# Optimization experiments

Hardware: AMD Instinct MI355X
Metric: run time of the kernel (lower is better)

## Reference

```python
import jax, jax.numpy as jnp
import numpy as np

N, H2, T = 64, 1024, 512  # num steps/documents, 2*hidden_dim, tokens per step
EPS = 1e-12  # torch F.normalize eps


def setup_inputs() -> dict:
    key = jax.random.key(0)
    k1, k2, k3, k4 = jax.random.split(key, 4)
    return {
        "hidden_states": jax.random.normal(k1, (N, H2, T), dtype=jnp.float32),
        "W_attention": jax.random.normal(k2, (H2, H2), dtype=jnp.float32),
        "bias_attention": jax.random.normal(k3, (H2,), dtype=jnp.float32),
        "u_w0": jax.random.normal(k4, (H2,), dtype=jnp.float32),
    }


def reference(hidden_states, W_attention, bias_attention, u_w0):
    n = hidden_states.shape[0]

    # Sequential recurrence on u_w: u_w <- normalize(u_w @ W^T + b), updated
    # BEFORE being used at each step i. Collect the post-update value per step.
    def step(u, _):
        u_new = u @ W_attention.T + bias_attention
        u_new = u_new / jnp.maximum(jnp.linalg.norm(u_new), EPS)
        return u_new, u_new

    _, u_ws = jax.lax.scan(step, u_w0, None, length=n)  # (N, 2H)

    # u_it = tanh(h_i^T W^T + b) for all steps, batched: (N, T, 2H)
    u_it = jnp.tanh(jnp.einsum('ndt,ed->nte', hidden_states, W_attention)
                    + bias_attention)

    # attention scores per step, softmax over the T axis (torch Softmax(dim=0)
    # on a (T,1) column)
    scores = jnp.einsum('nte,ne->nt', u_it, u_ws)  # (N, T)
    a = jax.nn.softmax(scores, axis=1)

    # weighted sum s_i = h_i @ a_i -> stacked as rows: (N, 2H)
    s = jnp.einsum('ndt,nt->nd', hidden_states, a)
    return s
```

## Files before the change

kernel.cpp:

```cpp
#include <hip/hip_runtime.h>
#include <cstdint>
#include <cstddef>

#define H2 1024
#define TT 512
#define NSTEPS 64
#define RBLK 32
#define RTHR 512
#define PREBLK 224
#define TOTBLK 256
#define NTILES 2048u
#define NOUT 512u

using floatx4 = __attribute__((__ext_vector_type__(4))) float;
using half8   = __attribute__((__ext_vector_type__(8))) _Float16;
using half4   = __attribute__((__ext_vector_type__(4))) _Float16;
typedef unsigned long long u64;

__device__ __forceinline__ float tanh_fast(float x) {
  return 1.0f - 2.0f / (__expf(2.0f * x) + 1.0f);
}

#define GLDS16(gp, lp)                                                         \
  __builtin_amdgcn_global_load_lds(                                            \
      (const __attribute__((address_space(1))) void*)(gp),                     \
      (__attribute__((address_space(3))) void*)(lp), 16, 0, 0)

__global__ __launch_bounds__(RTHR, 1) void fused_kernel(
    const float* __restrict__ W, const float* __restrict__ bias,
    const float* __restrict__ u0, float* __restrict__ vbuf,
    float* __restrict__ norm2, _Float16* __restrict__ Wh,
    const float* __restrict__ h, _Float16* __restrict__ hhT,
    float* __restrict__ scores, float* __restrict__ out,
    unsigned* __restrict__ ctrs) {
  __shared__ __align__(16) char smem[98432];
  int tid = threadIdx.x;
  unsigned* done    = ctrs;
  unsigned* queue   = ctrs + 16;
  unsigned* donecnt = ctrs + 32;
  unsigned* outq    = ctrs + 96;

  if (blockIdx.x < RBLK) {
    float* ub = (float*)smem;
    float* bredn = (float*)(smem + 8192);
    int w = tid >> 6, l = tid & 63;
    int r0 = blockIdx.x * RBLK + w * 4;

    floatx4 wreg[16];
    float blv[4];
#pragma unroll
    for (int p = 0; p < 4; ++p) {
      const float* wr = W + ((size_t)(r0 + p) << 10) + 4 * l;
#pragma unroll
      for (int j = 0; j < 4; ++j)
        wreg[p * 4 + j] = *(const floatx4*)(wr + 256 * j);
      blv[p] = bias[r0 + p];
    }
#pragma unroll
    for (int j = 0; j < 16; ++j) asm volatile("" : "+v"(wreg[j]));

    for (int i = 0; i < NSTEPS; ++i) {
      float* cb = ub + (i & 1) * 1024;
      float rs;
      if (i == 0) {
        if (w == 0) {
#pragma unroll
          for (int j = 0; j < 4; ++j) {
            floatx4 v = *((const floatx4*)u0 + l + 64 * j);
            *(floatx4*)(cb + 4 * l + 256 * j) = v;
          }
        }
        __syncthreads();
        rs = 1.0f;
      } else {
        if (w == 0) {
          const u64* src = (const u64*)(vbuf + ((size_t)(i - 1) << 10)) + l;
          u64 v[8];
          for (;;) {
            bool ok = true;
#pragma unroll
            for (int j = 0; j < 8; ++j) {
              v[j] = __hip_atomic_load(src + 64 * j, __ATOMIC_RELAXED,
                                       __HIP_MEMORY_SCOPE_AGENT);
              ok &= ((unsigned)(v[j] & 0xFFFFFFFFu) != 0xFFFFFFFFu) &
                    ((unsigned)(v[j] >> 32) != 0xFFFFFFFFu);
            }
            if (__all(ok)) break;
            __builtin_amdgcn_s_sleep(1);
          }
          float sq = 0.f;
#pragma unroll
          for (int j = 0; j < 8; ++j) {
            *(u64*)(cb + 2 * l + 128 * j) = v[j];
            float f0 =
                __builtin_bit_cast(float, (unsigned)(v[j] & 0xFFFFFFFFu));
            float f1 = __builtin_bit_cast(float, (unsigned)(v[j] >> 32));
            sq += f0 * f0 + f1 * f1;
          }
#pragma unroll
          for (int off = 1; off <= 32; off <<= 1)
            sq += __shfl_xor(sq, off, 64);
          if (l == 0) bredn[i & 1] = sq;
        }
        __syncthreads();
        float nrm = bredn[i & 1];
        rs = 1.0f / fmaxf(sqrtf(nrm), 1e-12f);
        if (blockIdx.x == 0 && tid == 64) {
          unsigned nb = __builtin_bit_cast(unsigned, nrm);
          __hip_atomic_store((unsigned*)(norm2 + (i - 1)), nb,
                             __ATOMIC_RELAXED, __HIP_MEMORY_SCOPE_AGENT);
        }
      }

      float acc0 = 0.f, acc1 = 0.f, acc2 = 0.f, acc3 = 0.f;
#pragma unroll
      for (int j = 0; j < 4; ++j) {
        floatx4 zv = *(const floatx4*)(cb + 256 * j + 4 * l);
        floatx4 w0 = wreg[0 * 4 + j], w1 = wreg[1 * 4 + j];
        floatx4 w2v = wreg[2 * 4 + j], w3 = wreg[3 * 4 + j];
        acc0 += w0.x * zv.x + w0.y * zv.y + w0.z * zv.z + w0.w * zv.w;
        acc1 += w1.x * zv.x + w1.y * zv.y + w1.z * zv.z + w1.w * zv.w;
        acc2 += w2v.x * zv.x + w2v.y * zv.y + w2v.z * zv.z + w2v.w * zv.w;
        acc3 += w3.x * zv.x + w3.y * zv.y + w3.z * zv.z + w3.w * zv.w;
      }
#pragma unroll
      for (int off = 1; off <= 32; off <<= 1) {
        acc0 += __shfl_xor(acc0, off, 64);
        acc1 += __shfl_xor(acc1, off, 64);
        acc2 += __shfl_xor(acc2, off, 64);
        acc3 += __shfl_xor(acc3, off, 64);
      }
      if (l == 0) {
        float y0 = acc0 * rs + blv[0], y1 = acc1 * rs + blv[1];
        float y2 = acc2 * rs + blv[2], y3 = acc3 * rs + blv[3];
        u64 a01 = ((u64)__builtin_bit_cast(unsigned, y1) << 32) |
                  (u64)__builtin_bit_cast(unsigned, y0);
        u64 a23 = ((u64)__builtin_bit_cast(unsigned, y3) << 32) |
                  (u64)__builtin_bit_cast(unsigned, y2);
        u64* dst = (u64*)(vbuf + ((size_t)i << 10) + r0);
        __hip_atomic_store(dst, a01, __ATOMIC_RELAXED,
                           __HIP_MEMORY_SCOPE_AGENT);
        __hip_atomic_store(dst + 1, a23, __ATOMIC_RELAXED,
                           __HIP_MEMORY_SCOPE_AGENT);
      }
    }

    if (blockIdx.x == 0 && (tid >> 6) == 0) {
      int l2 = tid & 63;
      const u64* src = (const u64*)(vbuf + ((size_t)(NSTEPS - 1) << 10)) + l2;
      u64 v[8];
      for (;;) {
        bool ok = true;
#pragma unroll
        for (int j = 0; j < 8; ++j) {
          v[j] = __hip_atomic_load(src + 64 * j, __ATOMIC_RELAXED,
                                   __HIP_MEMORY_SCOPE_AGENT);
          ok &= ((unsigned)(v[j] & 0xFFFFFFFFu) != 0xFFFFFFFFu) &
                ((unsigned)(v[j] >> 32) != 0xFFFFFFFFu);
        }
        if (__all(ok)) break;
        __builtin_amdgcn_s_sleep(1);
      }
      float sq = 0.f;
#pragma unroll
      for (int j = 0; j < 8; ++j) {
        float f0 = __builtin_bit_cast(float, (unsigned)(v[j] & 0xFFFFFFFFu));
        float f1 = __builtin_bit_cast(float, (unsigned)(v[j] >> 32));
        sq += f0 * f0 + f1 * f1;
      }
#pragma unroll
      for (int off = 1; off <= 32; off <<= 1) sq += __shfl_xor(sq, off, 64);
      if (l2 == 0) {
        unsigned nb = __builtin_bit_cast(unsigned, sq);
        __hip_atomic_store((unsigned*)(norm2 + (NSTEPS - 1)), nb,
                           __ATOMIC_RELAXED, __HIP_MEMORY_SCOPE_AGENT);
      }
    }
    __syncthreads();
  } else {
    int pb = blockIdx.x - RBLK;

    const floatx4* Wv = (const floatx4*)W;
    for (int idx = pb * RTHR + tid; idx < H2 * H2 / 4; idx += PREBLK * RTHR) {
      floatx4 v = Wv[idx];
      half4 o = {(_Float16)v.x, (_Float16)v.y, (_Float16)v.z, (_Float16)v.w};
      __hip_atomic_store((u64*)Wh + idx, __builtin_bit_cast(u64, o),
                         __ATOMIC_RELAXED, __HIP_MEMORY_SCOPE_AGENT);
    }

    int sub = tid >> 8, ltid = tid & 255;
    float(*tile)[65] = (float(*)[65])(smem + sub * 16640);
    int dr = ltid >> 4, tc = (ltid & 15) << 2;
    int tr = ltid >> 3, seg = ltid & 7;
    for (int base = pb * 2; base < 8192; base += PREBLK * 2) {
      int tidx = base + sub;
      bool act = tidx < 8192;
      int n = tidx >> 7, rem = tidx & 127;
      int d0 = (rem & 15) << 6, t0 = ((rem >> 4) & 7) << 6;
      if (act) {
        const float* hb = h + ((size_t)n * H2 + d0) * TT + t0;
#pragma unroll
        for (int p = 0; p < 4; ++p) {
          floatx4 v = *(const floatx4*)(hb + (size_t)(dr + p * 16) * TT + tc);
          tile[dr + p * 16][tc] = v.x;
          tile[dr + p * 16][tc + 1] = v.y;
          tile[dr + p * 16][tc + 2] = v.z;
          tile[dr + p * 16][tc + 3] = v.w;
        }
      }
      __syncthreads();
      if (act) {
        _Float16* ob = hhT + ((size_t)n * TT + t0) * H2 + d0;
#pragma unroll
        for (int p = 0; p < 2; ++p) {
          int t = tr + p * 32;
          union { half8 v; u64 u[2]; } hu;
#pragma unroll
          for (int u = 0; u < 8; ++u) hu.v[u] = (_Float16)tile[seg * 8 + u][t];
          u64* op = (u64*)(ob + (size_t)t * H2 + seg * 8);
          __hip_atomic_store(op, hu.u[0], __ATOMIC_RELAXED,
                             __HIP_MEMORY_SCOPE_AGENT);
          __hip_atomic_store(op + 1, hu.u[1], __ATOMIC_RELAXED,
                             __HIP_MEMORY_SCOPE_AGENT);
        }
      }
      __syncthreads();
    }
    asm volatile("s_waitcnt vmcnt(0)" ::: "memory");
    __syncthreads();
    if (tid == 0)
      __hip_atomic_fetch_add(done, 1u, __ATOMIC_RELEASE,
                             __HIP_MEMORY_SCOPE_AGENT);
  }

  if (tid == 0) {
    while (__hip_atomic_load(done, __ATOMIC_ACQUIRE,
                             __HIP_MEMORY_SCOPE_AGENT) < (unsigned)PREBLK)
      __builtin_amdgcn_s_sleep(2);
  }
  __syncthreads();

  int half = tid >> 8, tid2 = tid & 255;
  _Float16* Hsh = (_Float16*)(smem) + half * 24576;
  unsigned* tslot = (unsigned*)(smem + 98304);

  int lane = tid2 & 63, w2 = tid2 >> 6;
  int q = lane >> 4, m = lane & 15;
  int eoff = (w2 & 1) * 64, toff = (w2 >> 1) * 64;
  int rl = lane >> 2, kseg = lane & 3;
  int ksegx = kseg ^ (rl & 3);
  int xq = q ^ (m & 3);

  for (;;) {
    if (tid == 0) {
      unsigned q0 = atomicAdd(queue, 2u);
      tslot[0] = q0;
      tslot[1] = q0 + 1u;
    }
    __syncthreads();
    if (tslot[0] >= NTILES) break;
    unsigned tau = tslot[half];
    int n = (int)(tau >> 5);
    int rem = (int)(tau & 31u);
    int e_base = (rem & 7) << 7, t_base = (rem >> 3) << 7;

    const _Float16* gA0 =
        Wh + (((size_t)(e_base + w2 * 32 + rl)) << 10) + ksegx * 8;
    const _Float16* gA1 = gA0 + ((size_t)16 << 10);
    const _Float16* gB0 = hhT + ((size_t)n << 19) +
                          (((size_t)(t_base + w2 * 32 + rl)) << 10) + ksegx * 8;
    const _Float16* gB1 = gB0 + ((size_t)16 << 10);

    floatx4 zero = {0.f, 0.f, 0.f, 0.f};
    floatx4 acc[4][4];
#pragma unroll
    for (int i = 0; i < 4; ++i)
#pragma unroll
      for (int j = 0; j < 4; ++j) acc[i][j] = zero;

    {
      _Float16* b0 = Hsh + (w2 * 32) * 32;
      GLDS16(gA0, b0);
      GLDS16(gA1, b0 + 512);
      GLDS16(gB0, b0 + 4096);
      GLDS16(gB1, b0 + 4096 + 512);
      _Float16* b1 = Hsh + 8192 + (w2 * 32) * 32;
      GLDS16(gA0 + 32, b1);
      GLDS16(gA1 + 32, b1 + 512);
      GLDS16(gB0 + 32, b1 + 4096);
      GLDS16(gB1 + 32, b1 + 4096 + 512);
    }
#pragma unroll 1
    for (int kk = 0; kk < 32; ++kk) {
      if (kk < 31)
        asm volatile("s_waitcnt vmcnt(4)" ::: "memory");
      else
        asm volatile("s_waitcnt vmcnt(0)" ::: "memory");
      __builtin_amdgcn_s_barrier();
      __builtin_amdgcn_sched_barrier(0);
      const _Float16* Abuf = Hsh + (kk % 3) * 8192;
      const _Float16* Bbuf = Abuf + 4096;
      half8 af[4], bf[4];
#pragma unroll
      for (int i = 0; i < 4; ++i)
        af[i] = *(const half8*)&Abuf[(eoff + i * 16 + m) * 32 + xq * 8];
#pragma unroll
      for (int j = 0; j < 4; ++j)
        bf[j] = *(const half8*)&Bbuf[(toff + j * 16 + m) * 32 + xq * 8];
      if (kk + 2 < 32) {
        _Float16* nb = Hsh + ((kk + 2) % 3) * 8192 + (w2 * 32) * 32;
        GLDS16(gA0 + (kk + 2) * 32, nb);
        GLDS16(gA1 + (kk + 2) * 32, nb + 512);
        GLDS16(gB0 + (kk + 2) * 32, nb + 4096);
        GLDS16(gB1 + (kk + 2) * 32, nb + 4096 + 512);
      }
      __builtin_amdgcn_sched_barrier(0);
#pragma unroll
      for (int i = 0; i < 4; ++i)
#pragma unroll
        for (int j = 0; j < 4; ++j)
          acc[i][j] = __builtin_amdgcn_mfma_f32_16x16x32_f16(af[i], bf[j],
                                                             acc[i][j], 0, 0, 0);
    }
    __syncthreads();

    float* uloc = (float*)Hsh;
    float* bloc = uloc + 128;
    if (tid2 < 128) {
      float nn;
      for (;;) {
        unsigned b = __hip_atomic_load((const unsigned*)(norm2 + n),
                                       __ATOMIC_RELAXED,
                                       __HIP_MEMORY_SCOPE_AGENT);
        if (b != 0xFFFFFFFFu) {
          nn = __builtin_bit_cast(float, b);
          break;
        }
        __builtin_amdgcn_s_sleep(1);
      }
      float rsn = 1.0f / fmaxf(sqrtf(nn), 1e-12f);
      const unsigned* vp =
          (const unsigned*)(vbuf + ((size_t)n << 10) + e_base) + tid2;
      float vv;
      for (;;) {
        unsigned b =
            __hip_atomic_load(vp, __ATOMIC_RELAXED, __HIP_MEMORY_SCOPE_AGENT);
        if (b != 0xFFFFFFFFu) {
          vv = __builtin_bit_cast(float, b);
          break;
        }
        __builtin_amdgcn_s_sleep(1);
      }
      uloc[tid2] = vv * rsn;
      bloc[tid2] = bias[e_base + tid2];
    }
    __syncthreads();

    float part[4] = {0.f, 0.f, 0.f, 0.f};
#pragma unroll
    for (int i = 0; i < 4; ++i) {
#pragma unroll
      for (int reg = 0; reg < 4; ++reg) {
        int el = eoff + i * 16 + q * 4 + reg;
        float ubv = uloc[el];
        float bbv = bloc[el];
#pragma unroll
        for (int j = 0; j < 4; ++j) {
          float y = acc[i][j][reg] + bbv;
          part[j] += tanh_fast(y) * ubv;
        }
      }
    }
#pragma unroll
    for (int j = 0; j < 4; ++j) {
      part[j] += __shfl_xor(part[j], 16, 64);
      part[j] += __shfl_xor(part[j], 32, 64);
      if (lane < 16) {
        int t = t_base + toff + j * 16 + lane;
        atomicAdd(&scores[(size_t)n * TT + t], part[j]);
      }
    }
    __syncthreads();
    if (tid2 == 0)
      __hip_atomic_fetch_add(donecnt + n, 1u, __ATOMIC_RELEASE,
                             __HIP_MEMORY_SCOPE_AGENT);
  }

  {
    float* sa = (float*)smem;
    float* red = sa + 512;
    unsigned* oslot = (unsigned*)(sa + 528);
    int w = tid >> 6, lane = tid & 63;

    for (;;) {
      if (tid == 0) *oslot = atomicAdd(outq, 1u);
      __syncthreads();
      unsigned u = *oslot;
      if (u >= NOUT) break;
      int n = (int)(u >> 3), dblk = (int)(u & 7u);

      if (tid == 0) {
        while (__hip_atomic_load(donecnt + n, __ATOMIC_ACQUIRE,
                                 __HIP_MEMORY_SCOPE_AGENT) < 32u)
          __builtin_amdgcn_s_sleep(1);
      }
      __syncthreads();

      float s = __builtin_bit_cast(
          float, __hip_atomic_load((const unsigned*)(scores + (size_t)n * TT) +
                                       tid,
                                   __ATOMIC_RELAXED, __HIP_MEMORY_SCOPE_AGENT));
      float mx = s;
#pragma unroll
      for (int off = 32; off >= 1; off >>= 1)
        mx = fmaxf(mx, __shfl_xor(mx, off, 64));
      if (lane == 0) red[w] = mx;
      __syncthreads();
      mx = red[0];
#pragma unroll
      for (int k2 = 1; k2 < 8; ++k2) mx = fmaxf(mx, red[k2]);
      float e = __expf(s - mx);
      float ssum = e;
#pragma unroll
      for (int off = 32; off >= 1; off >>= 1) ssum += __shfl_xor(ssum, off, 64);
      if (lane == 0) red[8 + w] = ssum;
      __syncthreads();
      ssum = 0.f;
#pragma unroll
      for (int k2 = 0; k2 < 8; ++k2) ssum += red[8 + k2];
      sa[tid] = e * (1.0f / ssum);
      __syncthreads();

      int d0 = dblk * 128 + w * 16;
      const float4* hb =
          reinterpret_cast<const float4*>(h + (size_t)n * H2 * TT);
#pragma unroll 1
      for (int rr = 0; rr < 16; ++rr) {
        int d = d0 + rr;
        const float4* hr = hb + (size_t)d * (TT / 4);
        float4 a4 = hr[lane];
        float4 b4 = hr[64 + lane];
        int t0 = 4 * lane;
        float acc = a4.x * sa[t0] + a4.y * sa[t0 + 1] + a4.z * sa[t0 + 2] +
                    a4.w * sa[t0 + 3] + b4.x * sa[256 + t0] +
                    b4.y * sa[256 + t0 + 1] + b4.z * sa[256 + t0 + 2] +
                    b4.w * sa[256 + t0 + 3];
#pragma unroll
        for (int off = 1; off <= 32; off <<= 1) acc += __shfl_xor(acc, off, 64);
        if (lane == 0) out[(size_t)n * H2 + d] = acc;
      }
      __syncthreads();
    }
  }
}

extern "C" void kernel_launch(void* const* d_in, const int* in_sizes, int n_in,
                              void* d_out, int out_size, void* d_ws, size_t ws_size,
                              hipStream_t stream) {
  const float* h    = (const float*)d_in[0];
  const float* W    = (const float*)d_in[1];
  const float* bias = (const float*)d_in[2];
  const float* u0   = (const float*)d_in[3];
  float* out = (float*)d_out;

  float* wsf    = (float*)d_ws;
  float* norm2  = wsf;
  float* scores = wsf + 64;
  float* vbuf   = wsf + 64 + NSTEPS * TT;
  unsigned* ctrs = (unsigned*)(vbuf + (size_t)NSTEPS * H2);
  float* after = (float*)(ctrs + 128);
  _Float16* Wh  = (_Float16*)after;
  _Float16* hhT = Wh + (size_t)H2 * H2;

  hipMemsetAsync(norm2, 0xFF, 64 * sizeof(float), stream);
  hipMemsetAsync(scores, 0, (size_t)NSTEPS * TT * sizeof(float), stream);
  hipMemsetAsync(vbuf, 0xFF, (size_t)NSTEPS * H2 * sizeof(float), stream);
  hipMemsetAsync(ctrs, 0, 128 * sizeof(unsigned), stream);

  {
    const float* Wp = W; const float* bp = bias; const float* up = u0;
    float* vp = vbuf; float* np = norm2;
    _Float16* whp = Wh; const float* hp = h; _Float16* htp = hhT;
    float* sp = scores; float* op = out; unsigned* cp = ctrs;
    void* kargs[] = {&Wp, &bp, &up, &vp, &np, &whp, &hp, &htp, &sp, &op, &cp};
    hipLaunchCooperativeKernel((void*)fused_kernel, dim3(TOTBLK), dim3(RTHR),
                               kargs, 0, stream);
  }

  (void)in_sizes; (void)n_in; (void)out_size; (void)ws_size;
}
```

Baseline: 504.0 us.

## Fuse fp16 conversion and transpose into GEMM tile loads, drop pre-pass

Removes the separate pre-pass that converted W to fp16 and transposed hidden_states into an fp16 workspace before the GEMM. Each GEMM tile now reads fp32 W and h directly, converts to fp16 in registers and writes into LDS, which cuts the extra global write and re-read of the converted copies and the global barrier waiting for the pre-pass. In exchange it drops the async global-to-LDS triple-buffered pipeline for a single-buffered load, sync and compute loop, so load latency is no longer hidden. The B tile is also transposed through scalar LDS stores that may bank-conflict, and the memsets are merged.

```diff
diff --git a/kernel.cpp b/kernel.cpp
--- a/kernel.cpp
+++ b/kernel.cpp
@@ -7,36 +7,27 @@
 #define NSTEPS 64
 #define RBLK 32
 #define RTHR 512
-#define PREBLK 224
 #define TOTBLK 256
 #define NTILES 2048u
 #define NOUT 512u
 
 using floatx4 = __attribute__((__ext_vector_type__(4))) float;
 using half8   = __attribute__((__ext_vector_type__(8))) _Float16;
-using half4   = __attribute__((__ext_vector_type__(4))) _Float16;
 typedef unsigned long long u64;
 
 __device__ __forceinline__ float tanh_fast(float x) {
   return 1.0f - 2.0f / (__expf(2.0f * x) + 1.0f);
 }
 
-#define GLDS16(gp, lp)                                                         \
-  __builtin_amdgcn_global_load_lds(                                            \
-      (const __attribute__((address_space(1))) void*)(gp),                     \
-      (__attribute__((address_space(3))) void*)(lp), 16, 0, 0)
-
 __global__ __launch_bounds__(RTHR, 1) void fused_kernel(
     const float* __restrict__ W, const float* __restrict__ bias,
     const float* __restrict__ u0, float* __restrict__ vbuf,
-    float* __restrict__ norm2, _Float16* __restrict__ Wh,
-    const float* __restrict__ h, _Float16* __restrict__ hhT,
+    float* __restrict__ norm2, const float* __restrict__ h,
     float* __restrict__ scores, float* __restrict__ out,
     unsigned* __restrict__ ctrs) {
-  __shared__ __align__(16) char smem[98432];
+  __shared__ __align__(16) char smem[33792];
   int tid = threadIdx.x;
-  unsigned* done    = ctrs;
-  unsigned* queue   = ctrs + 16;
+  unsigned* gemmq   = ctrs + 16;
   unsigned* donecnt = ctrs + 32;
   unsigned* outq    = ctrs + 96;
 
@@ -177,83 +168,23 @@
       }
     }
     __syncthreads();
-  } else {
-    int pb = blockIdx.x - RBLK;
-
-    const floatx4* Wv = (const floatx4*)W;
-    for (int idx = pb * RTHR + tid; idx < H2 * H2 / 4; idx += PREBLK * RTHR) {
-      floatx4 v = Wv[idx];
-      half4 o = {(_Float16)v.x, (_Float16)v.y, (_Float16)v.z, (_Float16)v.w};
-      __hip_atomic_store((u64*)Wh + idx, __builtin_bit_cast(u64, o),
-                         __ATOMIC_RELAXED, __HIP_MEMORY_SCOPE_AGENT);
-    }
-
-    int sub = tid >> 8, ltid = tid & 255;
-    float(*tile)[65] = (float(*)[65])(smem + sub * 16640);
-    int dr = ltid >> 4, tc = (ltid & 15) << 2;
-    int tr = ltid >> 3, seg = ltid & 7;
-    for (int base = pb * 2; base < 8192; base += PREBLK * 2) {
-      int tidx = base + sub;
-      bool act = tidx < 8192;
-      int n = tidx >> 7, rem = tidx & 127;
-      int d0 = (rem & 15) << 6, t0 = ((rem >> 4) & 7) << 6;
-      if (act) {
-        const float* hb = h + ((size_t)n * H2 + d0) * TT + t0;
-#pragma unroll
-        for (int p = 0; p < 4; ++p) {
-          floatx4 v = *(const floatx4*)(hb + (size_t)(dr + p * 16) * TT + tc);
-          tile[dr + p * 16][tc] = v.x;
-          tile[dr + p * 16][tc + 1] = v.y;
-          tile[dr + p * 16][tc + 2] = v.z;
-          tile[dr + p * 16][tc + 3] = v.w;
-        }
-      }
-      __syncthreads();
-      if (act) {
-        _Float16* ob = hhT + ((size_t)n * TT + t0) * H2 + d0;
-#pragma unroll
-        for (int p = 0; p < 2; ++p) {
-          int t = tr + p * 32;
-          union { half8 v; u64 u[2]; } hu;
-#pragma unroll
-          for (int u = 0; u < 8; ++u) hu.v[u] = (_Float16)tile[seg * 8 + u][t];
-          u64* op = (u64*)(ob + (size_t)t * H2 + seg * 8);
-          __hip_atomic_store(op, hu.u[0], __ATOMIC_RELAXED,
-                             __HIP_MEMORY_SCOPE_AGENT);
-          __hip_atomic_store(op + 1, hu.u[1], __ATOMIC_RELAXED,
-                             __HIP_MEMORY_SCOPE_AGENT);
-        }
-      }
-      __syncthreads();
-    }
-    asm volatile("s_waitcnt vmcnt(0)" ::: "memory");
-    __syncthreads();
-    if (tid == 0)
-      __hip_atomic_fetch_add(done, 1u, __ATOMIC_RELEASE,
-                             __HIP_MEMORY_SCOPE_AGENT);
   }
 
-  if (tid == 0) {
-    while (__hip_atomic_load(done, __ATOMIC_ACQUIRE,
-                             __HIP_MEMORY_SCOPE_AGENT) < (unsigned)PREBLK)
-      __builtin_amdgcn_s_sleep(2);
-  }
-  __syncthreads();
-
   int half = tid >> 8, tid2 = tid & 255;
-  _Float16* Hsh = (_Float16*)(smem) + half * 24576;
-  unsigned* tslot = (unsigned*)(smem + 98304);
+  _Float16* Ash = (_Float16*)(smem + half * 16384);
+  _Float16* Bsh = Ash + 4096;
+  unsigned* tslot = (unsigned*)(smem + 32768);
+  float* nnsh = (float*)(smem + 32776);
 
   int lane = tid2 & 63, w2 = tid2 >> 6;
   int q = lane >> 4, m = lane & 15;
   int eoff = (w2 & 1) * 64, toff = (w2 >> 1) * 64;
-  int rl = lane >> 2, kseg = lane & 3;
-  int ksegx = kseg ^ (rl & 3);
-  int xq = q ^ (m & 3);
+  int ar = tid2 >> 1, as = (tid2 & 1) * 16;
+  int bk = tid2 & 31, bt = (tid2 >> 5) * 16;
 
   for (;;) {
     if (tid == 0) {
-      unsigned q0 = atomicAdd(queue, 2u);
+      unsigned q0 = atomicAdd(gemmq, 2u);
       tslot[0] = q0;
       tslot[1] = q0 + 1u;
     }
@@ -264,12 +195,9 @@
     int rem = (int)(tau & 31u);
     int e_base = (rem & 7) << 7, t_base = (rem >> 3) << 7;
 
-    const _Float16* gA0 =
-        Wh + (((size_t)(e_base + w2 * 32 + rl)) << 10) + ksegx * 8;
-    const _Float16* gA1 = gA0 + ((size_t)16 << 10);
-    const _Float16* gB0 = hhT + ((size_t)n << 19) +
-                          (((size_t)(t_base + w2 * 32 + rl)) << 10) + ksegx * 8;
-    const _Float16* gB1 = gB0 + ((size_t)16 << 10);
+    const float* Arow = W + ((size_t)(e_base + ar) << 10) + as;
+    const float* Brow =
+        h + ((size_t)n << 19) + ((size_t)bk << 9) + t_base + bt;
 
     floatx4 zero = {0.f, 0.f, 0.f, 0.f};
     floatx4 acc[4][4];
@@ -278,80 +206,72 @@
 #pragma unroll
       for (int j = 0; j < 4; ++j) acc[i][j] = zero;
 
-    {
-      _Float16* b0 = Hsh + (w2 * 32) * 32;
-      GLDS16(gA0, b0);
-      GLDS16(gA1, b0 + 512);
-      GLDS16(gB0, b0 + 4096);
-      GLDS16(gB1, b0 + 4096 + 512);
-      _Float16* b1 = Hsh + 8192 + (w2 * 32) * 32;
-      GLDS16(gA0 + 32, b1);
-      GLDS16(gA1 + 32, b1 + 512);
-      GLDS16(gB0 + 32, b1 + 4096);
-      GLDS16(gB1 + 32, b1 + 4096 + 512);
-    }
-#pragma unroll 1
-    for (int kk = 0; kk < 32; ++kk) {
-      if (kk < 31)
-        asm volatile("s_waitcnt vmcnt(4)" ::: "memory");
-      else
-        asm volatile("s_waitcnt vmcnt(0)" ::: "memory");
-      __builtin_amdgcn_s_barrier();
-      __builtin_amdgcn_sched_barrier(0);
-      const _Float16* Abuf = Hsh + (kk % 3) * 8192;
-      const _Float16* Bbuf = Abuf + 4096;
+    for (int k0 = 0; k0 < H2; k0 += 32) {
+      floatx4 a0 = *(const floatx4*)(Arow + k0);
+      floatx4 a1 = *(const floatx4*)(Arow + k0 + 4);
+      floatx4 a2 = *(const floatx4*)(Arow + k0 + 8);
+      floatx4 a3 = *(const floatx4*)(Arow + k0 + 12);
+      half8 h0, h1;
+#pragma unroll
+      for (int c = 0; c < 4; ++c) {
+        h0[c] = (_Float16)a0[c];
+        h0[4 + c] = (_Float16)a1[c];
+        h1[c] = (_Float16)a2[c];
+        h1[4 + c] = (_Float16)a3[c];
+      }
+      *(half8*)&Ash[ar * 32 + as] = h0;
+      *(half8*)&Ash[ar * 32 + as + 8] = h1;
+
+      floatx4 b0 = *(const floatx4*)(Brow + (size_t)k0 * TT);
+      floatx4 b1 = *(const floatx4*)(Brow + (size_t)k0 * TT + 4);
+      floatx4 b2 = *(const floatx4*)(Brow + (size_t)k0 * TT + 8);
+      floatx4 b3 = *(const floatx4*)(Brow + (size_t)k0 * TT + 12);
+#pragma unroll
+      for (int c = 0; c < 4; ++c) {
+        Bsh[(bt + c) * 32 + bk] = (_Float16)b0[c];
+        Bsh[(bt + 4 + c) * 32 + bk] = (_Float16)b1[c];
+        Bsh[(bt + 8 + c) * 32 + bk] = (_Float16)b2[c];
+        Bsh[(bt + 12 + c) * 32 + bk] = (_Float16)b3[c];
+      }
+      __syncthreads();
+
       half8 af[4], bf[4];
 #pragma unroll
       for (int i = 0; i < 4; ++i)
-        af[i] = *(const half8*)&Abuf[(eoff + i * 16 + m) * 32 + xq * 8];
+        af[i] = *(const half8*)&Ash[(eoff + i * 16 + m) * 32 + q * 8];
 #pragma unroll
       for (int j = 0; j < 4; ++j)
-        bf[j] = *(const half8*)&Bbuf[(toff + j * 16 + m) * 32 + xq * 8];
-      if (kk + 2 < 32) {
-        _Float16* nb = Hsh + ((kk + 2) % 3) * 8192 + (w2 * 32) * 32;
-        GLDS16(gA0 + (kk + 2) * 32, nb);
-        GLDS16(gA1 + (kk + 2) * 32, nb + 512);
-        GLDS16(gB0 + (kk + 2) * 32, nb + 4096);
-        GLDS16(gB1 + (kk + 2) * 32, nb + 4096 + 512);
-      }
-      __builtin_amdgcn_sched_barrier(0);
+        bf[j] = *(const half8*)&Bsh[(toff + j * 16 + m) * 32 + q * 8];
 #pragma unroll
       for (int i = 0; i < 4; ++i)
 #pragma unroll
         for (int j = 0; j < 4; ++j)
           acc[i][j] = __builtin_amdgcn_mfma_f32_16x16x32_f16(af[i], bf[j],
                                                              acc[i][j], 0, 0, 0);
-    }
-    __syncthreads();
-
-    float* uloc = (float*)Hsh;
+      __syncthreads();
+    }
+
+    float* uloc = (float*)Ash;
     float* bloc = uloc + 128;
-    if (tid2 < 128) {
-      float nn;
+    if (tid2 == 0) {
       for (;;) {
         unsigned b = __hip_atomic_load((const unsigned*)(norm2 + n),
                                        __ATOMIC_RELAXED,
                                        __HIP_MEMORY_SCOPE_AGENT);
         if (b != 0xFFFFFFFFu) {
-          nn = __builtin_bit_cast(float, b);
+          nnsh[half] = __builtin_bit_cast(float, b);
           break;
         }
-        __builtin_amdgcn_s_sleep(1);
-      }
-      float rsn = 1.0f / fmaxf(sqrtf(nn), 1e-12f);
-      const unsigned* vp =
-          (const unsigned*)(vbuf + ((size_t)n << 10) + e_base) + tid2;
-      float vv;
-      for (;;) {
-        unsigned b =
-            __hip_atomic_load(vp, __ATOMIC_RELAXED, __HIP_MEMORY_SCOPE_AGENT);
-        if (b != 0xFFFFFFFFu) {
-          vv = __builtin_bit_cast(float, b);
-          break;
-        }
-        __builtin_amdgcn_s_sleep(1);
-      }
-      uloc[tid2] = vv * rsn;
+        __builtin_amdgcn_s_sleep(4);
+      }
+    }
+    __syncthreads();
+    float rsn = 1.0f / fmaxf(sqrtf(nnsh[half]), 1e-12f);
+    if (tid2 < 128) {
+      unsigned b = __hip_atomic_load(
+          (const unsigned*)(vbuf + ((size_t)n << 10) + e_base) + tid2,
+          __ATOMIC_RELAXED, __HIP_MEMORY_SCOPE_AGENT);
+      uloc[tid2] = __builtin_bit_cast(float, b) * rsn;
       bloc[tid2] = bias[e_base + tid2];
     }
     __syncthreads();
@@ -390,12 +310,13 @@
     float* sa = (float*)smem;
     float* red = sa + 512;
     unsigned* oslot = (unsigned*)(sa + 528);
-    int w = tid >> 6, lane = tid & 63;
+    int w = tid >> 6, lane2 = tid & 63;
 
     for (;;) {
       if (tid == 0) *oslot = atomicAdd(outq, 1u);
       __syncthreads();
       unsigned u = *oslot;
+      __syncthreads();
       if (u >= NOUT) break;
       int n = (int)(u >> 3), dblk = (int)(u & 7u);
 
@@ -414,7 +335,7 @@
 #pragma unroll
       for (int off = 32; off >= 1; off >>= 1)
         mx = fmaxf(mx, __shfl_xor(mx, off, 64));
-      if (lane == 0) red[w] = mx;
+      if (lane2 == 0) red[w] = mx;
       __syncthreads();
       mx = red[0];
 #pragma unroll
@@ -423,7 +344,7 @@
       float ssum = e;
 #pragma unroll
       for (int off = 32; off >= 1; off >>= 1) ssum += __shfl_xor(ssum, off, 64);
-      if (lane == 0) red[8 + w] = ssum;
+      if (lane2 == 0) red[8 + w] = ssum;
       __syncthreads();
       ssum = 0.f;
 #pragma unroll
@@ -438,16 +359,16 @@
       for (int rr = 0; rr < 16; ++rr) {
         int d = d0 + rr;
         const float4* hr = hb + (size_t)d * (TT / 4);
-        float4 a4 = hr[lane];
-        float4 b4 = hr[64 + lane];
-        int t0 = 4 * lane;
+        float4 a4 = hr[lane2];
+        float4 b4 = hr[64 + lane2];
+        int t0 = 4 * lane2;
         float acc = a4.x * sa[t0] + a4.y * sa[t0 + 1] + a4.z * sa[t0 + 2] +
                     a4.w * sa[t0 + 3] + b4.x * sa[256 + t0] +
                     b4.y * sa[256 + t0 + 1] + b4.z * sa[256 + t0 + 2] +
                     b4.w * sa[256 + t0 + 3];
 #pragma unroll
         for (int off = 1; off <= 32; off <<= 1) acc += __shfl_xor(acc, off, 64);
-        if (lane == 0) out[(size_t)n * H2 + d] = acc;
+        if (lane2 == 0) out[(size_t)n * H2 + d] = acc;
       }
       __syncthreads();
     }
@@ -465,24 +386,18 @@
 
   float* wsf    = (float*)d_ws;
   float* norm2  = wsf;
-  float* scores = wsf + 64;
-  float* vbuf   = wsf + 64 + NSTEPS * TT;
-  unsigned* ctrs = (unsigned*)(vbuf + (size_t)NSTEPS * H2);
-  float* after = (float*)(ctrs + 128);
-  _Float16* Wh  = (_Float16*)after;
-  _Float16* hhT = Wh + (size_t)H2 * H2;
-
-  hipMemsetAsync(norm2, 0xFF, 64 * sizeof(float), stream);
-  hipMemsetAsync(scores, 0, (size_t)NSTEPS * TT * sizeof(float), stream);
-  hipMemsetAsync(vbuf, 0xFF, (size_t)NSTEPS * H2 * sizeof(float), stream);
-  hipMemsetAsync(ctrs, 0, 128 * sizeof(unsigned), stream);
+  float* vbuf   = wsf + 64;
+  float* scores = wsf + 64 + (size_t)NSTEPS * H2;
+  unsigned* ctrs = (unsigned*)(scores + (size_t)NSTEPS * TT);
+
+  hipMemsetAsync(norm2, 0xFF, (64 + (size_t)NSTEPS * H2) * 4, stream);
+  hipMemsetAsync(scores, 0, ((size_t)NSTEPS * TT + 128) * 4, stream);
 
   {
     const float* Wp = W; const float* bp = bias; const float* up = u0;
-    float* vp = vbuf; float* np = norm2;
-    _Float16* whp = Wh; const float* hp = h; _Float16* htp = hhT;
+    float* vp = vbuf; float* np = norm2; const float* hp = h;
     float* sp = scores; float* op = out; unsigned* cp = ctrs;
-    void* kargs[] = {&Wp, &bp, &up, &vp, &np, &whp, &hp, &htp, &sp, &op, &cp};
+    void* kargs[] = {&Wp, &bp, &up, &vp, &np, &hp, &sp, &op, &cp};
     hipLaunchCooperativeKernel((void*)fused_kernel, dim3(TOTBLK), dim3(RTHR),
                                kargs, 0, stream);
   }
```

New measurement: 637.7 us. 1.27x slower.
